# Kernel tuning notes

Measured on AMD Instinct MI355X. Metric: run time of the kernel, lower is better.

Reference implementation:

```python
import jax, jax.numpy as jnp
import numpy as np

N, E = 10000, 160000
DIN, H, DOUT, DE = 128, 256, 256, 32


def _lin(k, din, dout, scale=0.05):
    return jax.random.normal(k, (din, dout), jnp.float32) * scale


def setup_inputs() -> dict:
    key = jax.random.key(0)
    ks = jax.random.split(key, 40)
    inp = {}
    inp["x"] = jax.random.normal(ks[0], (N, DIN), jnp.float32)
    inp["edge_attr"] = jax.random.normal(ks[1], (E, DE), jnp.float32)
    inp["src"] = jax.random.randint(ks[2], (E,), 0, N, jnp.int32)
    inp["dst"] = jax.random.randint(ks[3], (E,), 0, N, jnp.int32)
    # encoders
    inp["W_edge_enc"] = _lin(ks[4], DE, H); inp["b_edge_enc"] = jnp.zeros((H,), jnp.float32)
    inp["W_node_enc"] = _lin(ks[5], DIN, H); inp["b_node_enc"] = jnp.zeros((H,), jnp.float32)
    # 3 TransformerConv layers (heads=1): q,k,v (with bias), edge (no bias), skip (with bias)
    outs = [H, H, DOUT]
    i = 6
    for l, C in enumerate(outs, start=1):
        inp[f"Wq{l}"] = _lin(ks[i], H, C); i += 1
        inp[f"bq{l}"] = jnp.zeros((C,), jnp.float32)
        inp[f"Wk{l}"] = _lin(ks[i], H, C); i += 1
        inp[f"bk{l}"] = jnp.zeros((C,), jnp.float32)
        inp[f"Wv{l}"] = _lin(ks[i], H, C); i += 1
        inp[f"bv{l}"] = jnp.zeros((C,), jnp.float32)
        inp[f"We{l}"] = _lin(ks[i], H, C); i += 1
        inp[f"Ws{l}"] = _lin(ks[i], H, C); i += 1
        inp[f"bs{l}"] = jnp.zeros((C,), jnp.float32)
    return inp


def _tconv(x, src, dst, edge_emb, Wq, bq, Wk, bk, Wv, bv, We, Ws, bs):
    # PyG TransformerConv, heads=1, concat=True, root_weight=True
    n = x.shape[0]
    C = Wq.shape[1]
    q = x @ Wq + bq            # [N, C]
    k = x @ Wk + bk            # [N, C]
    v = x @ Wv + bv            # [N, C]
    e = edge_emb @ We          # [E, C] (lin_edge, no bias)
    kj = k[src] + e            # [E, C]
    alpha = jnp.sum(q[dst] * kj, axis=-1) / jnp.sqrt(jnp.float32(C))  # [E]
    # segment softmax over incoming edges per target node
    m = jax.ops.segment_max(alpha, dst, num_segments=n)
    a = jnp.exp(alpha - m[dst])
    denom = jax.ops.segment_sum(a, dst, num_segments=n)
    a = a / jnp.maximum(denom[dst], 1e-16)
    msg = (v[src] + e) * a[:, None]                       # [E, C]
    out = jax.ops.segment_sum(msg, dst, num_segments=n)   # [N, C]
    return out + x @ Ws + bs                               # root skip


def reference(x, edge_attr, src, dst,
              W_edge_enc, b_edge_enc, W_node_enc, b_node_enc,
              Wq1, bq1, Wk1, bk1, Wv1, bv1, We1, Ws1, bs1,
              Wq2, bq2, Wk2, bk2, Wv2, bv2, We2, Ws2, bs2,
              Wq3, bq3, Wk3, bk3, Wv3, bv3, We3, Ws3, bs3):
    relu = jax.nn.relu
    edge_feat = relu(edge_attr @ W_edge_enc + b_edge_enc)  # [E, H]
    h = relu(x @ W_node_enc + b_node_enc)                  # [N, H]
    # dropout(0.3) is identity in eval mode
    h = relu(_tconv(h, src, dst, edge_feat, Wq1, bq1, Wk1, bk1, Wv1, bv1, We1, Ws1, bs1))
    h = relu(_tconv(h, src, dst, edge_feat, Wq2, bq2, Wk2, bk2, Wv2, bv2, We2, Ws2, bs2))
    h = _tconv(h, src, dst, edge_feat, Wq3, bq3, Wk3, bk3, Wv3, bv3, We3, Ws3, bs3)
    return h
```

## Files before the change

kernel.cpp:

```cpp
#include <hip/hip_runtime.h>
#include <cstdint>

typedef unsigned short u16;
typedef __attribute__((ext_vector_type(8))) short short8;
typedef __attribute__((ext_vector_type(8))) __bf16 bf16x8;
typedef __attribute__((ext_vector_type(4))) float f32x4;

#define DEV __device__ __forceinline__

DEV u16 f2bf(float f){
  uint32_t u = __float_as_uint(f);
  u += 0x7fffu + ((u >> 16) & 1u);
  return (u16)(u >> 16);
}
DEV float bf2f(u16 h){ return __uint_as_float(((uint32_t)h) << 16); }

DEV f32x4 mfma16(short8 a, short8 b, f32x4 c){
  return __builtin_amdgcn_mfma_f32_16x16x32_bf16(
      __builtin_bit_cast(bf16x8, a), __builtin_bit_cast(bf16x8, b), c, 0, 0, 0);
}

#define NN 10000
#define EE 160000
#define MPN 10112
#define MPE 160128

__global__ void count_k(const int* __restrict__ dst, int* __restrict__ cnt){
  int i = blockIdx.x * 256 + threadIdx.x;
  if(i < EE) atomicAdd(&cnt[dst[i]], 1);
}

__global__ void scan1_k(const int* __restrict__ cnt, int* __restrict__ offs,
                        int* __restrict__ bsum){
  __shared__ int buf[256];
  int b = blockIdx.x, tid = threadIdx.x, i = b * 256 + tid;
  int v = (i < NN) ? cnt[i] : 0;
  buf[tid] = v; __syncthreads();
  for(int d = 1; d < 256; d <<= 1){
    int t = (tid >= d) ? buf[tid - d] : 0;
    __syncthreads();
    buf[tid] += t;
    __syncthreads();
  }
  if(i < NN) offs[i] = buf[tid] - v;
  if(tid == 255) bsum[b] = buf[255];
}

__global__ void scan23_k(int* __restrict__ offs, const int* __restrict__ bsum,
                         int* __restrict__ cursor){
  __shared__ int bpre_s;
  int b = blockIdx.x, tid = threadIdx.x;
  if(tid == 0){
    int s = 0;
    for(int i = 0; i < b; ++i) s += bsum[i];
    bpre_s = s;
  }
  __syncthreads();
  int i = b * 256 + tid;
  if(i < NN){ int v = offs[i] + bpre_s; offs[i] = v; cursor[i] = v; }
  if(i == 0) offs[NN] = EE;
}

__global__ void scatter_k(const int* __restrict__ dst, int* __restrict__ cursor,
                          int* __restrict__ eids){
  int i = blockIdx.x * 256 + threadIdx.x;
  if(i < EE){ int p = atomicAdd(&cursor[dst[i]], 1); eids[p] = i; }
}

__global__ void rank_k(const int* __restrict__ dst, const int* __restrict__ src,
                       const int* __restrict__ offs, const int* __restrict__ eids,
                       int* __restrict__ eidp, int* __restrict__ srcp){
  int e = blockIdx.x * 256 + threadIdx.x;
  if(e >= MPE) return;
  if(e >= EE){ eidp[e] = e; return; }
  int n = dst[e];
  int p0 = offs[n], p1 = offs[n + 1];
  int rk = 0;
  for(int p = p0; p < p1; ++p) rk += (eids[p] < e) ? 1 : 0;
  int slot = p0 + rk;
  eidp[slot] = e;
  srcp[slot] = src[e];
}

struct WPack {
  const float* Wq[3]; const float* Wk[3]; const float* Wv[3];
  const float* Ws[3]; const float* We[3];
  const float* bq[3]; const float* bk[3]; const float* bv[3]; const float* bs[3];
};

#define PG0 5056
#define PG1 (PG0 + 20016)
#define PG2 (PG1 + 3840)
#define PG3 (PG2 + 1536)
#define PG4 (PG3 + 15)
#define PG5 (PG4 + 256)

__global__ __launch_bounds__(256) void prep_all_k(
    const float* __restrict__ x, const float* __restrict__ eattr, WPack P,
    const float* __restrict__ Wne, const float* __restrict__ Wee,
    u16* __restrict__ xbf, u16* __restrict__ eabf,
    u16* __restrict__ Wcat, u16* __restrict__ Wet,
    u16* __restrict__ WqBF, u16* __restrict__ WeBF,
    float* __restrict__ biasc, u16* __restrict__ Wnet, u16* __restrict__ Weet)
{
  int b = blockIdx.x, tid = threadIdx.x;
  if(b < PG0){
    int i = b * 256 + tid;
    xbf[i] = (i < NN * 128) ? f2bf(x[i]) : (u16)0;
  } else if(b < PG1){
    int i = (b - PG0) * 256 + tid;
    eabf[i] = (i < EE * 32) ? f2bf(eattr[i]) : (u16)0;
  } else if(b < PG2){
    int b2 = b - PG1; int l = b2 / 1280, r = b2 % 1280; int k = tid;
    float v;
    if(r < 256)       v = P.Wq[l][k * 256 + r];
    else if(r < 512)  v = P.Ws[l][k * 256 + (r - 256)];
    else if(r < 768){ Wet[((size_t)l * 256 + (r - 512)) * 256 + k] =
                        f2bf(P.We[l][k * 256 + (r - 512)]); return; }
    else if(r < 1024) v = P.Wk[l][k * 256 + (r - 768)];
    else              v = P.Wv[l][k * 256 + (r - 1024)];
    Wcat[((size_t)l * 1280 + r) * 256 + k] = f2bf(v);
  } else if(b < PG3){
    int b3 = b - PG2; int l = b3 >> 9, rr = b3 & 511; int t = tid;
    if(rr < 256) WqBF[((size_t)l * 256 + rr) * 256 + t] = f2bf(P.Wq[l][rr * 256 + t]);
    else         WeBF[((size_t)l * 256 + (rr - 256)) * 256 + t] = f2bf(P.We[l][(rr - 256) * 256 + t]);
  } else if(b < PG4){
    int b4 = b - PG3; int l = b4 / 5, seg = b4 % 5; int t = tid;
    float v;
    if(seg == 0)      v = P.bq[l][t];
    else if(seg == 1) v = P.bs[l][t];
    else if(seg == 2){
      const float* we = P.We[l] + (size_t)t * 256; const float* bq = P.bq[l];
      float s = 0.f;
      for(int c = 0; c < 256; ++c) s += bq[c] * we[c];
      v = s;
    }
    else if(seg == 3) v = P.bk[l][t];
    else              v = P.bv[l][t];
    biasc[(size_t)l * 1280 + seg * 256 + t] = v;
  } else {
    int n = b - PG4;
    if(tid < 128) Wnet[n * 128 + tid] = f2bf(Wne[(size_t)tid * 256 + n]);
    if(tid < 32)  Weet[n * 32 + tid]  = f2bf(Wee[(size_t)tid * 256 + n]);
  }
}

template<int BK, int EPI, int AG = 0>
__global__ __launch_bounds__(256) void gemm_k(
    const u16* __restrict__ A, const u16* __restrict__ Bt,
    const float* __restrict__ bias, void* __restrict__ Out,
    const float* __restrict__ accv, const float* __restrict__ skipS,
    const int* __restrict__ rowmap, u16* __restrict__ kvout,
    float* __restrict__ skipOut,
    int Mreal, int Nld, int K, size_t sA, size_t sB, size_t sOb)
{
  constexpr int CPR = BK / 8;
  constexpr int SW  = (BK == 64) ? 7 : 3;
  __shared__ short8 smem8[2048];
  u16* Al = (u16*)smem8;
  u16* Bl = Al + 128 * BK;
  A  += (size_t)blockIdx.z * sA;
  Bt += (size_t)blockIdx.z * sB;
  Out = (void*)((char*)Out + (size_t)blockIdx.z * sOb);
  int tid = threadIdx.x, lane = tid & 63;
  int rowBase = blockIdx.x * 128, colBase = blockIdx.y * 128;
  int wave = tid >> 6, wm = wave >> 1, wn = wave & 1;
  int lr = lane & 15, lk = lane >> 4;
  f32x4 acc[4][4] = {};
  int nkt = K / BK;
  for(int kt = 0; kt < nkt; ++kt){
    __syncthreads();
    for(int ci = tid; ci < 128 * CPR; ci += 256){
      int r = ci / CPR, cb = ci % CPR;
      int ar = AG ? rowmap[rowBase + r] : (rowBase + r);
      int d = (r * CPR + (cb ^ (r & SW))) * 8;
      *(short8*)&Al[d] = *(const short8*)&A [(size_t)ar * K + kt * BK + cb * 8];
      *(short8*)&Bl[d] = *(const short8*)&Bt[(size_t)(colBase + r) * K + kt * BK + cb * 8];
    }
    __syncthreads();
    #pragma unroll
    for(int kk = 0; kk < BK / 32; ++kk){
      short8 af[4], bfr[4];
      #pragma unroll
      for(int m = 0; m < 4; ++m){
        int r = wm * 64 + m * 16 + lr;
        int byt = r * (BK * 2) + kk * 64 + lk * 16; byt ^= (r & SW) << 4;
        af[m] = *(const short8*)((const char*)Al + byt);
      }
      #pragma unroll
      for(int n = 0; n < 4; ++n){
        int r = wn * 64 + n * 16 + lr;
        int byt = r * (BK * 2) + kk * 64 + lk * 16; byt ^= (r & SW) << 4;
        bfr[n] = *(const short8*)((const char*)Bl + byt);
      }
      #pragma unroll
      for(int m = 0; m < 4; ++m)
        #pragma unroll
        for(int n = 0; n < 4; ++n)
          acc[m][n] = mfma16(af[m], bfr[n], acc[m][n]);
    }
  }

  __syncthreads();
  if constexpr(EPI == 0){
    int sec = colBase >> 8;
    if(sec == 1){
      float* fs = (float*)smem8;
      #pragma unroll
      for(int h = 0; h < 2; ++h){
        if(wm == h){
          #pragma unroll
          for(int m = 0; m < 4; ++m)
            #pragma unroll
            for(int n = 0; n < 4; ++n){
              int cc = wn * 64 + n * 16 + lr;
              #pragma unroll
              for(int j = 0; j < 4; ++j){
                int r2 = m * 16 + lk * 4 + j;
                fs[r2 * 128 + cc] = acc[m][n][j] + bias[colBase + cc];
              }
            }
        }
        __syncthreads();
        for(int ch = tid; ch < 2048; ch += 256){
          int rr = ch >> 5, cc = (ch & 31) << 2;
          int r = rowBase + h * 64 + rr;
          if(r < Mreal)
            *(float4*)&skipOut[(size_t)r * 256 + (colBase - 256) + cc] = *(float4*)&fs[rr * 128 + cc];
        }
        __syncthreads();
      }
    } else {
      u16* us = (u16*)smem8;
      #pragma unroll
      for(int m = 0; m < 4; ++m)
        #pragma unroll
        for(int n = 0; n < 4; ++n){
          int cc = wn * 64 + n * 16 + lr;
          #pragma unroll
          for(int j = 0; j < 4; ++j){
            int rr = wm * 64 + m * 16 + lk * 4 + j;
            us[rr * 128 + cc] = f2bf(acc[m][n][j] + bias[colBase + cc]);
          }
        }
      __syncthreads();
      u16* dstp; int cofs;
      if(sec == 0){ dstp = (u16*)Out; cofs = colBase; }
      else if(sec == 2){ dstp = (u16*)Out; cofs = colBase - 256; }
      else { dstp = kvout; cofs = colBase - 768; }
      for(int ch = tid; ch < 2048; ch += 256){
        int rr = ch >> 4, cc = (ch & 15) << 3;
        int r = rowBase + rr;
        if(r < Mreal)
          *(short8*)&dstp[(size_t)r * 512 + cofs + cc] = *(short8*)&us[rr * 128 + cc];
      }
    }
  } else if constexpr(EPI == 4){
    float* fs = (float*)smem8;
    #pragma unroll
    for(int h = 0; h < 2; ++h){
      if(wm == h){
        #pragma unroll
        for(int m = 0; m < 4; ++m)
          #pragma unroll
          for(int n = 0; n < 4; ++n){
            int cc = wn * 64 + n * 16 + lr;
            int c = colBase + cc;
            #pragma unroll
            for(int j = 0; j < 4; ++j){
              int r2 = m * 16 + lk * 4 + j;
              int r = rowBase + h * 64 + r2;
              fs[r2 * 128 + cc] = acc[m][n][j]
                + accv[(size_t)r * 256 + c] + skipS[(size_t)r * 256 + c];
            }
          }
      }
      __syncthreads();
      for(int ch = tid; ch < 2048; ch += 256){
        int rr = ch >> 5, cc = (ch & 31) << 2;
        int r = rowBase + h * 64 + rr;
        if(r < Mreal)
          *(float4*)&((float*)Out)[(size_t)r * Nld + colBase + cc] = *(float4*)&fs[rr * 128 + cc];
      }
      __syncthreads();
    }
  } else {
    u16* us = (u16*)smem8;
    #pragma unroll
    for(int m = 0; m < 4; ++m)
      #pragma unroll
      for(int n = 0; n < 4; ++n){
        int cc = wn * 64 + n * 16 + lr;
        int c = colBase + cc;
        #pragma unroll
        for(int j = 0; j < 4; ++j){
          int rr = wm * 64 + m * 16 + lk * 4 + j;
          float v = acc[m][n][j];
          if constexpr(EPI == 1){ v += bias[c]; v = fmaxf(v, 0.f); }
          else if constexpr(EPI == 3){
            int r = rowBase + rr;
            v += accv[(size_t)r * 256 + c] + skipS[(size_t)r * 256 + c];
            v = fmaxf(v, 0.f);
          }
          us[rr * 128 + cc] = f2bf(v);
        }
      }
    __syncthreads();
    for(int ch = tid; ch < 2048; ch += 256){
      int rr = ch >> 4, cc = (ch & 15) << 3;
      int r = rowBase + rr;
      if(r < Mreal)
        *(short8*)&((u16*)Out)[(size_t)r * Nld + colBase + cc] = *(short8*)&us[rr * 128 + cc];
    }
  }
}

__global__ __launch_bounds__(256) void node_pass_k(
    const u16* __restrict__ qq, const u16* __restrict__ efp,
    const u16* __restrict__ kvbf,
    const int* __restrict__ srcp, const int* __restrict__ offs,
    float* __restrict__ accv, u16* __restrict__ aggef)
{
  int tid = threadIdx.x, lane = tid & 63;
  int li = lane & 15, gb = lane & 48;
  int n = blockIdx.x * 16 + (tid >> 4);
  if(n >= NN) return;
  const u16* qrow = qq + (size_t)n * 512 + li * 16;
  short8 qh0 = *(const short8*)(qrow),       qh1 = *(const short8*)(qrow + 8);
  short8 eh0 = *(const short8*)(qrow + 256), eh1 = *(const short8*)(qrow + 264);
  float q[16], e[16];
  #pragma unroll
  for(int d = 0; d < 8; ++d){
    q[d] = bf2f((u16)qh0[d]); q[8 + d] = bf2f((u16)qh1[d]);
    e[d] = bf2f((u16)eh0[d]); e[8 + d] = bf2f((u16)eh1[d]);
  }
  float av[16], ag[16];
  #pragma unroll
  for(int d = 0; d < 16; ++d){ av[d] = 0.f; ag[d] = 0.f; }
  float den = 0.f;
  int p0 = offs[n], deg = offs[n + 1] - p0;
  for(int base = 0; base < deg; base += 16){
    int scnt = deg - base; if(scnt > 16) scnt = 16;
    int ssrc = (li < scnt) ? srcp[p0 + base + li] : 0;
    int jj = 0;
    for(; jj + 1 < scnt; jj += 2){
      int s1 = __shfl(ssrc, gb + jj);
      int s2 = __shfl(ssrc, gb + jj + 1);
      size_t p1 = (size_t)(p0 + base + jj);
      const u16* kv1 = kvbf + ((size_t)s1 << 9) + li * 16;
      const u16* kv2 = kvbf + ((size_t)s2 << 9) + li * 16;
      const u16* e1 = efp + (p1 << 8) + li * 16;
      const u16* e2 = efp + ((p1 + 1) << 8) + li * 16;
      short8 kA1 = *(const short8*)(kv1),       kB1 = *(const short8*)(kv1 + 8);
      short8 vA1 = *(const short8*)(kv1 + 256), vB1 = *(const short8*)(kv1 + 264);
      short8 fA1 = *(const short8*)(e1),        fB1 = *(const short8*)(e1 + 8);
      short8 kA2 = *(const short8*)(kv2),       kB2 = *(const short8*)(kv2 + 8);
      short8 vA2 = *(const short8*)(kv2 + 256), vB2 = *(const short8*)(kv2 + 264);
      short8 fA2 = *(const short8*)(e2),        fB2 = *(const short8*)(e2 + 8);
      float sc1 = 0.f, sc2 = 0.f;
      #pragma unroll
      for(int d = 0; d < 8; ++d){
        sc1 += q[d]   * bf2f((u16)kA1[d]) + e[d]   * bf2f((u16)fA1[d]);
        sc1 += q[8+d] * bf2f((u16)kB1[d]) + e[8+d] * bf2f((u16)fB1[d]);
        sc2 += q[d]   * bf2f((u16)kA2[d]) + e[d]   * bf2f((u16)fA2[d]);
        sc2 += q[8+d] * bf2f((u16)kB2[d]) + e[8+d] * bf2f((u16)fB2[d]);
      }
      sc1 += __shfl_xor(sc1, 1); sc2 += __shfl_xor(sc2, 1);
      sc1 += __shfl_xor(sc1, 2); sc2 += __shfl_xor(sc2, 2);
      sc1 += __shfl_xor(sc1, 4); sc2 += __shfl_xor(sc2, 4);
      sc1 += __shfl_xor(sc1, 8); sc2 += __shfl_xor(sc2, 8);
      float w1 = __expf(sc1 * 0.0625f);
      float w2 = __expf(sc2 * 0.0625f);
      den += w1 + w2;
      #pragma unroll
      for(int d = 0; d < 8; ++d){
        av[d]   += w1 * bf2f((u16)vA1[d]) + w2 * bf2f((u16)vA2[d]);
        av[8+d] += w1 * bf2f((u16)vB1[d]) + w2 * bf2f((u16)vB2[d]);
        ag[d]   += w1 * bf2f((u16)fA1[d]) + w2 * bf2f((u16)fA2[d]);
        ag[8+d] += w1 * bf2f((u16)fB1[d]) + w2 * bf2f((u16)fB2[d]);
      }
    }
    if(jj < scnt){
      int s = __shfl(ssrc, gb + jj);
      size_t p = (size_t)(p0 + base + jj);
      const u16* kvp = kvbf + ((size_t)s << 9) + li * 16;
      const u16* ep = efp + (p << 8) + li * 16;
      short8 kA = *(const short8*)(kvp),       kB = *(const short8*)(kvp + 8);
      short8 vA = *(const short8*)(kvp + 256), vB = *(const short8*)(kvp + 264);
      short8 fA = *(const short8*)(ep),        fB = *(const short8*)(ep + 8);
      float part = 0.f;
      #pragma unroll
      for(int d = 0; d < 8; ++d){
        part += q[d]   * bf2f((u16)kA[d]) + e[d]   * bf2f((u16)fA[d]);
        part += q[8+d] * bf2f((u16)kB[d]) + e[8+d] * bf2f((u16)fB[d]);
      }
      part += __shfl_xor(part, 1);
      part += __shfl_xor(part, 2);
      part += __shfl_xor(part, 4);
      part += __shfl_xor(part, 8);
      float wgt = __expf(part * 0.0625f);
      den += wgt;
      #pragma unroll
      for(int d = 0; d < 8; ++d){
        av[d]   += wgt * bf2f((u16)vA[d]);
        av[8+d] += wgt * bf2f((u16)vB[d]);
        ag[d]   += wgt * bf2f((u16)fA[d]);
        ag[8+d] += wgt * bf2f((u16)fB[d]);
      }
    }
  }
  float rden = 1.f / fmaxf(den, 1e-16f);
  float* ao = accv + (size_t)n * 256 + li * 16;
  #pragma unroll
  for(int t = 0; t < 4; ++t){
    float4 o;
    o.x = av[t*4+0] * rden; o.y = av[t*4+1] * rden;
    o.z = av[t*4+2] * rden; o.w = av[t*4+3] * rden;
    *(float4*)(ao + t * 4) = o;
  }
  u16* go = aggef + (size_t)n * 256 + li * 16;
  #pragma unroll
  for(int t = 0; t < 2; ++t){
    short8 o;
    #pragma unroll
    for(int d = 0; d < 8; ++d) o[d] = (short)f2bf(ag[t*8+d] * rden);
    *(short8*)(go + t * 8) = o;
  }
}

extern "C" void kernel_launch(void* const* d_in, const int* in_sizes, int n_in,
                              void* d_out, int out_size, void* d_ws, size_t ws_size,
                              hipStream_t stream){
  const float* x     = (const float*)d_in[0];
  const float* eattr = (const float*)d_in[1];
  const int*   src   = (const int*)d_in[2];
  const int*   dst   = (const int*)d_in[3];
  const float* Wee   = (const float*)d_in[4];
  const float* bee   = (const float*)d_in[5];
  const float* Wne   = (const float*)d_in[6];
  const float* bne   = (const float*)d_in[7];
  WPack P;
  for(int l = 0; l < 3; ++l){
    const int b = 8 + l * 9;
    P.Wq[l] = (const float*)d_in[b + 0]; P.bq[l] = (const float*)d_in[b + 1];
    P.Wk[l] = (const float*)d_in[b + 2]; P.bk[l] = (const float*)d_in[b + 3];
    P.Wv[l] = (const float*)d_in[b + 4]; P.bv[l] = (const float*)d_in[b + 5];
    P.We[l] = (const float*)d_in[b + 6];
    P.Ws[l] = (const float*)d_in[b + 7]; P.bs[l] = (const float*)d_in[b + 8];
  }

  char* w = (char*)d_ws; size_t off = 0;
  auto alloc = [&](size_t bytes)->char*{
    char* p = w + off; off = (off + bytes + 255) & ~(size_t)255; return p;
  };
  u16*   Wcat  = (u16*)  alloc((size_t)3 * 1280 * 256 * 2);
  u16*   Wet   = (u16*)  alloc((size_t)3 * 256 * 256 * 2);
  u16*   WqBF  = (u16*)  alloc((size_t)3 * 256 * 256 * 2);
  u16*   WeBF  = (u16*)  alloc((size_t)3 * 256 * 256 * 2);
  float* biasc = (float*)alloc((size_t)3 * 1280 * 4);
  u16*   Wnet  = (u16*)  alloc((size_t)256 * 128 * 2);
  u16*   Weet  = (u16*)  alloc((size_t)256 * 32 * 2);
  u16*   xbf   = (u16*)  alloc((size_t)MPN * 128 * 2);
  u16*   eabf  = (u16*)  alloc((size_t)MPE * 32 * 2);
  u16*   hbf   = (u16*)  alloc((size_t)MPN * 256 * 2);
  u16*   qq    = (u16*)  alloc((size_t)MPN * 512 * 2);
  float* skipf = (float*)alloc((size_t)MPN * 256 * 4);
  u16*   kvbf  = (u16*)  alloc((size_t)MPN * 512 * 2);
  u16*   efp   = (u16*)  alloc((size_t)MPE * 256 * 2);
  int*   cnt   = (int*)  alloc((size_t)NN * 4);
  int*   offs  = (int*)  alloc((size_t)(NN + 1) * 4);
  int*   cursor= (int*)  alloc((size_t)NN * 4);
  int*   bsum  = (int*)  alloc((size_t)64 * 4);
  int*   eids  = (int*)  alloc((size_t)EE * 4);
  int*   eidp  = (int*)  alloc((size_t)MPE * 4);
  int*   srcp  = (int*)  alloc((size_t)EE * 4);
  float* accv  = (float*)alloc((size_t)MPN * 256 * 4);
  u16*   aggef = (u16*)  alloc((size_t)MPN * 256 * 2);
  if(off > ws_size) return;

  hipMemsetAsync(cnt, 0, (size_t)NN * 4, stream);
  count_k <<<(EE + 255) / 256, 256, 0, stream>>>(dst, cnt);
  scan1_k <<<40, 256, 0, stream>>>(cnt, offs, bsum);
  scan23_k<<<40, 256, 0, stream>>>(offs, bsum, cursor);
  scatter_k<<<(EE + 255) / 256, 256, 0, stream>>>(dst, cursor, eids);
  rank_k  <<<(MPE + 255) / 256, 256, 0, stream>>>(dst, src, offs, eids, eidp, srcp);

  prep_all_k<<<PG5, 256, 0, stream>>>(x, eattr, P, Wne, Wee,
      xbf, eabf, Wcat, Wet, WqBF, WeBF, biasc, Wnet, Weet);

  gemm_k<64,5><<<dim3(2, 2, 3), 256, 0, stream>>>(
      WeBF, WqBF, nullptr, Wcat + (size_t)512 * 256,
      nullptr, nullptr, nullptr, nullptr, nullptr, 256, 256, 256,
      (size_t)256 * 256, (size_t)256 * 256, (size_t)1280 * 256 * 2);

  gemm_k<64,1><<<dim3(MPN / 128, 2), 256, 0, stream>>>(
      xbf, Wnet, bne, hbf, nullptr, nullptr, nullptr, nullptr, nullptr,
      NN, 256, 128, 0, 0, 0);
  gemm_k<32,1,1><<<dim3(MPE / 128, 2), 256, 0, stream>>>(
      eabf, Weet, bee, efp, nullptr, nullptr, eidp, nullptr, nullptr,
      EE, 256, 32, 0, 0, 0);

  for(int l = 0; l < 3; ++l){
    gemm_k<64,0><<<dim3(MPN / 128, 10), 256, 0, stream>>>(
        hbf, Wcat + (size_t)l * 1280 * 256, biasc + (size_t)l * 1280, qq,
        nullptr, nullptr, nullptr, kvbf, skipf, NN, 512, 256, 0, 0, 0);
    node_pass_k<<<625, 256, 0, stream>>>(qq, efp, kvbf, srcp, offs, accv, aggef);
    if(l < 2)
      gemm_k<64,3><<<dim3(MPN / 128, 2), 256, 0, stream>>>(
          aggef, Wet + (size_t)l * 256 * 256, nullptr, hbf,
          accv, skipf, nullptr, nullptr, nullptr, NN, 256, 256, 0, 0, 0);
    else
      gemm_k<64,4><<<dim3(MPN / 128, 2), 256, 0, stream>>>(
          aggef, Wet + (size_t)l * 256 * 256, nullptr, d_out,
          accv, skipf, nullptr, nullptr, nullptr, NN, 256, 256, 0, 0, 0);
  }
}
```

Baseline: 359.7 us.

## Fuse CSR build and encoder GEMMs, store intermediates in fp16, widen node pass

Four kernels for CSR counting and scanning become one single-block kernel that builds a histogram and prefix sum in shared memory. The three encoder and weight-fold GEMM launches merge into one kernel. The skip and accumulated-value intermediates are stored as fp16 instead of fp32, which halves their memory traffic. The node pass now uses a full wave per node and splits edges across four lane groups, then reduces them with shuffles. The single-block CSR kernel serialises the histogram over all edges, and fp16 storage loses some precision.

New measurement: 414.0 us. 1.15x slower.

```diff
diff --git a/kernel.cpp b/kernel.cpp
--- a/kernel.cpp
+++ b/kernel.cpp
@@ -14,6 +14,8 @@
   return (u16)(u >> 16);
 }
 DEV float bf2f(u16 h){ return __uint_as_float(((uint32_t)h) << 16); }
+DEV u16 f2h(float f){ return __builtin_bit_cast(u16, (_Float16)f); }
+DEV float h2f(u16 h){ return (float)__builtin_bit_cast(_Float16, h); }
 
 DEV f32x4 mfma16(short8 a, short8 b, f32x4 c){
   return __builtin_amdgcn_mfma_f32_16x16x32_bf16(
@@ -25,40 +27,38 @@
 #define MPN 10112
 #define MPE 160128
 
-__global__ void count_k(const int* __restrict__ dst, int* __restrict__ cnt){
-  int i = blockIdx.x * 256 + threadIdx.x;
-  if(i < EE) atomicAdd(&cnt[dst[i]], 1);
-}
-
-__global__ void scan1_k(const int* __restrict__ cnt, int* __restrict__ offs,
-                        int* __restrict__ bsum){
-  __shared__ int buf[256];
-  int b = blockIdx.x, tid = threadIdx.x, i = b * 256 + tid;
-  int v = (i < NN) ? cnt[i] : 0;
-  buf[tid] = v; __syncthreads();
-  for(int d = 1; d < 256; d <<= 1){
-    int t = (tid >= d) ? buf[tid - d] : 0;
+__global__ __launch_bounds__(1024) void csr1_k(const int* __restrict__ dst,
+                                               int* __restrict__ offs,
+                                               int* __restrict__ cursor){
+  __shared__ int hist[NN];
+  __shared__ int psum[1024];
+  int tid = threadIdx.x;
+  for(int i = tid; i < NN; i += 1024) hist[i] = 0;
+  __syncthreads();
+  for(int i = tid; i < EE; i += 1024) atomicAdd(&hist[dst[i]], 1);
+  __syncthreads();
+  int base = tid * 10;
+  int s = 0;
+  #pragma unroll
+  for(int j = 0; j < 10; ++j){
+    int idx = base + j;
+    if(idx < NN){ int t = hist[idx]; hist[idx] = s; s += t; }
+  }
+  psum[tid] = s;
+  __syncthreads();
+  for(int d = 1; d < 1024; d <<= 1){
+    int t = (tid >= d) ? psum[tid - d] : 0;
     __syncthreads();
-    buf[tid] += t;
+    psum[tid] += t;
     __syncthreads();
   }
-  if(i < NN) offs[i] = buf[tid] - v;
-  if(tid == 255) bsum[b] = buf[255];
-}
-
-__global__ void scan23_k(int* __restrict__ offs, const int* __restrict__ bsum,
-                         int* __restrict__ cursor){
-  __shared__ int bpre_s;
-  int b = blockIdx.x, tid = threadIdx.x;
-  if(tid == 0){
-    int s = 0;
-    for(int i = 0; i < b; ++i) s += bsum[i];
-    bpre_s = s;
-  }
-  __syncthreads();
-  int i = b * 256 + tid;
-  if(i < NN){ int v = offs[i] + bpre_s; offs[i] = v; cursor[i] = v; }
-  if(i == 0) offs[NN] = EE;
+  int add = (tid > 0) ? psum[tid - 1] : 0;
+  #pragma unroll
+  for(int j = 0; j < 10; ++j){
+    int idx = base + j;
+    if(idx < NN){ int v = hist[idx] + add; offs[idx] = v; cursor[idx] = v; }
+  }
+  if(tid == 0) offs[NN] = EE;
 }
 
 __global__ void scatter_k(const int* __restrict__ dst, int* __restrict__ cursor,
@@ -145,25 +145,25 @@
   }
 }
 
-template<int BK, int EPI, int AG = 0>
-__global__ __launch_bounds__(256) void gemm_k(
+template<int BK, int EPI, int AG>
+DEV void gemm_body(short8* smem8,
     const u16* __restrict__ A, const u16* __restrict__ Bt,
-    const float* __restrict__ bias, void* __restrict__ Out,
-    const float* __restrict__ accv, const float* __restrict__ skipS,
+    const float* __restrict__ bias, void* Out,
+    const u16* __restrict__ accvH, const u16* __restrict__ skipH,
     const int* __restrict__ rowmap, u16* __restrict__ kvout,
-    float* __restrict__ skipOut,
+    u16* __restrict__ skipOut,
+    int bx, int by, int bz,
     int Mreal, int Nld, int K, size_t sA, size_t sB, size_t sOb)
 {
   constexpr int CPR = BK / 8;
   constexpr int SW  = (BK == 64) ? 7 : 3;
-  __shared__ short8 smem8[2048];
   u16* Al = (u16*)smem8;
   u16* Bl = Al + 128 * BK;
-  A  += (size_t)blockIdx.z * sA;
-  Bt += (size_t)blockIdx.z * sB;
-  Out = (void*)((char*)Out + (size_t)blockIdx.z * sOb);
+  A  += (size_t)bz * sA;
+  Bt += (size_t)bz * sB;
+  Out = (void*)((char*)Out + (size_t)bz * sOb);
   int tid = threadIdx.x, lane = tid & 63;
-  int rowBase = blockIdx.x * 128, colBase = blockIdx.y * 128;
+  int rowBase = bx * 128, colBase = by * 128;
   int wave = tid >> 6, wm = wave >> 1, wn = wave & 1;
   int lr = lane & 15, lk = lane >> 4;
   f32x4 acc[4][4] = {};
@@ -202,60 +202,7 @@
   }
 
   __syncthreads();
-  if constexpr(EPI == 0){
-    int sec = colBase >> 8;
-    if(sec == 1){
-      float* fs = (float*)smem8;
-      #pragma unroll
-      for(int h = 0; h < 2; ++h){
-        if(wm == h){
-          #pragma unroll
-          for(int m = 0; m < 4; ++m)
-            #pragma unroll
-            for(int n = 0; n < 4; ++n){
-              int cc = wn * 64 + n * 16 + lr;
-              #pragma unroll
-              for(int j = 0; j < 4; ++j){
-                int r2 = m * 16 + lk * 4 + j;
-                fs[r2 * 128 + cc] = acc[m][n][j] + bias[colBase + cc];
-              }
-            }
-        }
-        __syncthreads();
-        for(int ch = tid; ch < 2048; ch += 256){
-          int rr = ch >> 5, cc = (ch & 31) << 2;
-          int r = rowBase + h * 64 + rr;
-          if(r < Mreal)
-            *(float4*)&skipOut[(size_t)r * 256 + (colBase - 256) + cc] = *(float4*)&fs[rr * 128 + cc];
-        }
-        __syncthreads();
-      }
-    } else {
-      u16* us = (u16*)smem8;
-      #pragma unroll
-      for(int m = 0; m < 4; ++m)
-        #pragma unroll
-        for(int n = 0; n < 4; ++n){
-          int cc = wn * 64 + n * 16 + lr;
-          #pragma unroll
-          for(int j = 0; j < 4; ++j){
-            int rr = wm * 64 + m * 16 + lk * 4 + j;
-            us[rr * 128 + cc] = f2bf(acc[m][n][j] + bias[colBase + cc]);
-          }
-        }
-      __syncthreads();
-      u16* dstp; int cofs;
-      if(sec == 0){ dstp = (u16*)Out; cofs = colBase; }
-      else if(sec == 2){ dstp = (u16*)Out; cofs = colBase - 256; }
-      else { dstp = kvout; cofs = colBase - 768; }
-      for(int ch = tid; ch < 2048; ch += 256){
-        int rr = ch >> 4, cc = (ch & 15) << 3;
-        int r = rowBase + rr;
-        if(r < Mreal)
-          *(short8*)&dstp[(size_t)r * 512 + cofs + cc] = *(short8*)&us[rr * 128 + cc];
-      }
-    }
-  } else if constexpr(EPI == 4){
+  if constexpr(EPI == 4){
     float* fs = (float*)smem8;
     #pragma unroll
     for(int h = 0; h < 2; ++h){
@@ -271,7 +218,7 @@
               int r2 = m * 16 + lk * 4 + j;
               int r = rowBase + h * 64 + r2;
               fs[r2 * 128 + cc] = acc[m][n][j]
-                + accv[(size_t)r * 256 + c] + skipS[(size_t)r * 256 + c];
+                + h2f(accvH[(size_t)r * 256 + c]) + h2f(skipH[(size_t)r * 256 + c]);
             }
           }
       }
@@ -283,6 +230,33 @@
           *(float4*)&((float*)Out)[(size_t)r * Nld + colBase + cc] = *(float4*)&fs[rr * 128 + cc];
       }
       __syncthreads();
+    }
+  } else if constexpr(EPI == 0){
+    int sec = by >> 1;
+    u16* us = (u16*)smem8;
+    #pragma unroll
+    for(int m = 0; m < 4; ++m)
+      #pragma unroll
+      for(int n = 0; n < 4; ++n){
+        int cc = wn * 64 + n * 16 + lr;
+        #pragma unroll
+        for(int j = 0; j < 4; ++j){
+          int rr = wm * 64 + m * 16 + lk * 4 + j;
+          float v = acc[m][n][j] + bias[colBase + cc];
+          us[rr * 128 + cc] = (sec == 1) ? f2h(v) : f2bf(v);
+        }
+      }
+    __syncthreads();
+    u16* dstp; int cofs, ldd;
+    if(sec == 0){ dstp = (u16*)Out; cofs = colBase; ldd = 512; }
+    else if(sec == 1){ dstp = skipOut; cofs = colBase - 256; ldd = 256; }
+    else if(sec == 2){ dstp = (u16*)Out; cofs = colBase - 256; ldd = 512; }
+    else { dstp = kvout; cofs = colBase - 768; ldd = 512; }
+    for(int ch = tid; ch < 2048; ch += 256){
+      int rr = ch >> 4, cc = (ch & 15) << 3;
+      int r = rowBase + rr;
+      if(r < Mreal)
+        *(short8*)&dstp[(size_t)r * ldd + cofs + cc] = *(short8*)&us[rr * 128 + cc];
     }
   } else {
     u16* us = (u16*)smem8;
@@ -299,7 +273,7 @@
           if constexpr(EPI == 1){ v += bias[c]; v = fmaxf(v, 0.f); }
           else if constexpr(EPI == 3){
             int r = rowBase + rr;
-            v += accv[(size_t)r * 256 + c] + skipS[(size_t)r * 256 + c];
+            v += h2f(accvH[(size_t)r * 256 + c]) + h2f(skipH[(size_t)r * 256 + c]);
             v = fmaxf(v, 0.f);
           }
           us[rr * 128 + cc] = f2bf(v);
@@ -315,16 +289,64 @@
   }
 }
 
+__global__ __launch_bounds__(256) void slab_k(
+    const u16* __restrict__ A, const u16* __restrict__ Bt,
+    const float* __restrict__ bias, u16* __restrict__ qq,
+    u16* __restrict__ kvout, u16* __restrict__ skipOut){
+  __shared__ short8 smem[2048];
+  gemm_body<64,0,0>(smem, A, Bt, bias, qq, nullptr, nullptr, nullptr, kvout, skipOut,
+                    blockIdx.x, blockIdx.y, 0, NN, 512, 256, 0, 0, 0);
+}
+
+__global__ __launch_bounds__(256) void out3_k(
+    const u16* __restrict__ A, const u16* __restrict__ Bt, u16* __restrict__ Out,
+    const u16* __restrict__ accvH, const u16* __restrict__ skipH){
+  __shared__ short8 smem[2048];
+  gemm_body<64,3,0>(smem, A, Bt, nullptr, Out, accvH, skipH, nullptr, nullptr, nullptr,
+                    blockIdx.x, blockIdx.y, 0, NN, 256, 256, 0, 0, 0);
+}
+
+__global__ __launch_bounds__(256) void out4_k(
+    const u16* __restrict__ A, const u16* __restrict__ Bt, float* __restrict__ Out,
+    const u16* __restrict__ accvH, const u16* __restrict__ skipH){
+  __shared__ short8 smem[2048];
+  gemm_body<64,4,0>(smem, A, Bt, nullptr, Out, accvH, skipH, nullptr, nullptr, nullptr,
+                    blockIdx.x, blockIdx.y, 0, NN, 256, 256, 0, 0, 0);
+}
+
+__global__ __launch_bounds__(256) void enc_all_k(
+    const u16* __restrict__ xbf, const u16* __restrict__ Wnet,
+    const float* __restrict__ bne, u16* __restrict__ hbf,
+    const u16* __restrict__ eabf, const u16* __restrict__ Weet,
+    const float* __restrict__ bee, u16* __restrict__ efp, const int* __restrict__ eidp,
+    const u16* __restrict__ WeBF, const u16* __restrict__ WqBF, u16* __restrict__ WcatQ){
+  __shared__ short8 smem[2048];
+  int b = blockIdx.x;
+  if(b < 158){
+    gemm_body<64,1,0>(smem, xbf, Wnet, bne, hbf, nullptr, nullptr, nullptr, nullptr, nullptr,
+                      b >> 1, b & 1, 0, NN, 256, 128, 0, 0, 0);
+  } else if(b < 2660){
+    int bb = b - 158;
+    gemm_body<32,1,1>(smem, eabf, Weet, bee, efp, nullptr, nullptr, eidp, nullptr, nullptr,
+                      bb >> 1, bb & 1, 0, EE, 256, 32, 0, 0, 0);
+  } else {
+    int bb = b - 2660;
+    gemm_body<64,5,0>(smem, WeBF, WqBF, nullptr, WcatQ, nullptr, nullptr, nullptr, nullptr, nullptr,
+                      bb & 1, (bb >> 1) & 1, bb >> 2, 256, 256, 256,
+                      (size_t)256 * 256, (size_t)256 * 256, (size_t)1280 * 256 * 2);
+  }
+}
+
 __global__ __launch_bounds__(256) void node_pass_k(
     const u16* __restrict__ qq, const u16* __restrict__ efp,
     const u16* __restrict__ kvbf,
     const int* __restrict__ srcp, const int* __restrict__ offs,
-    float* __restrict__ accv, u16* __restrict__ aggef)
+    u16* __restrict__ accvH, u16* __restrict__ aggef)
 {
-  int tid = threadIdx.x, lane = tid & 63;
-  int li = lane & 15, gb = lane & 48;
-  int n = blockIdx.x * 16 + (tid >> 4);
+  int wave = threadIdx.x >> 6, lane = threadIdx.x & 63;
+  int n = blockIdx.x * 4 + wave;
   if(n >= NN) return;
+  int li = lane & 15, eg = lane >> 4, gb = lane & 48;
   const u16* qrow = qq + (size_t)n * 512 + li * 16;
   short8 qh0 = *(const short8*)(qrow),       qh1 = *(const short8*)(qrow + 8);
   short8 eh0 = *(const short8*)(qrow + 256), eh1 = *(const short8*)(qrow + 264);
@@ -339,18 +361,21 @@
   for(int d = 0; d < 16; ++d){ av[d] = 0.f; ag[d] = 0.f; }
   float den = 0.f;
   int p0 = offs[n], deg = offs[n + 1] - p0;
-  for(int base = 0; base < deg; base += 16){
-    int scnt = deg - base; if(scnt > 16) scnt = 16;
-    int ssrc = (li < scnt) ? srcp[p0 + base + li] : 0;
+  int nwin = (deg + 63) >> 6;
+  for(int t = 0; t < nwin; ++t){
+    int gstart = t * 64 + eg * 16;
+    int rem = deg - gstart;
+    int scnt = rem < 16 ? (rem < 0 ? 0 : rem) : 16;
+    int ssrc = (li < scnt) ? srcp[p0 + gstart + li] : 0;
     int jj = 0;
     for(; jj + 1 < scnt; jj += 2){
       int s1 = __shfl(ssrc, gb + jj);
       int s2 = __shfl(ssrc, gb + jj + 1);
-      size_t p1 = (size_t)(p0 + base + jj);
+      size_t pp = (size_t)(p0 + gstart + jj);
       const u16* kv1 = kvbf + ((size_t)s1 << 9) + li * 16;
       const u16* kv2 = kvbf + ((size_t)s2 << 9) + li * 16;
-      const u16* e1 = efp + (p1 << 8) + li * 16;
-      const u16* e2 = efp + ((p1 + 1) << 8) + li * 16;
+      const u16* e1 = efp + (pp << 8) + li * 16;
+      const u16* e2 = efp + ((pp + 1) << 8) + li * 16;
       short8 kA1 = *(const short8*)(kv1),       kB1 = *(const short8*)(kv1 + 8);
       short8 vA1 = *(const short8*)(kv1 + 256), vB1 = *(const short8*)(kv1 + 264);
       short8 fA1 = *(const short8*)(e1),        fB1 = *(const short8*)(e1 + 8);
@@ -382,9 +407,9 @@
     }
     if(jj < scnt){
       int s = __shfl(ssrc, gb + jj);
-      size_t p = (size_t)(p0 + base + jj);
+      size_t pp = (size_t)(p0 + gstart + jj);
       const u16* kvp = kvbf + ((size_t)s << 9) + li * 16;
-      const u16* ep = efp + (p << 8) + li * 16;
+      const u16* ep = efp + (pp << 8) + li * 16;
       short8 kA = *(const short8*)(kvp),       kB = *(const short8*)(kvp + 8);
       short8 vA = *(const short8*)(kvp + 256), vB = *(const short8*)(kvp + 264);
       short8 fA = *(const short8*)(ep),        fB = *(const short8*)(ep + 8);
@@ -409,22 +434,31 @@
       }
     }
   }
+  #pragma unroll
+  for(int d = 0; d < 16; ++d){
+    av[d] += __shfl_xor(av[d], 16); av[d] += __shfl_xor(av[d], 32);
+    ag[d] += __shfl_xor(ag[d], 16); ag[d] += __shfl_xor(ag[d], 32);
+  }
+  den += __shfl_xor(den, 16); den += __shfl_xor(den, 32);
   float rden = 1.f / fmaxf(den, 1e-16f);
-  float* ao = accv + (size_t)n * 256 + li * 16;
-  #pragma unroll
-  for(int t = 0; t < 4; ++t){
-    float4 o;
-    o.x = av[t*4+0] * rden; o.y = av[t*4+1] * rden;
-    o.z = av[t*4+2] * rden; o.w = av[t*4+3] * rden;
-    *(float4*)(ao + t * 4) = o;
-  }
-  u16* go = aggef + (size_t)n * 256 + li * 16;
-  #pragma unroll
-  for(int t = 0; t < 2; ++t){
-    short8 o;
+  if(eg == 0){
+    u16* ao = accvH + (size_t)n * 256 + li * 16;
     #pragma unroll
-    for(int d = 0; d < 8; ++d) o[d] = (short)f2bf(ag[t*8+d] * rden);
-    *(short8*)(go + t * 8) = o;
+    for(int t = 0; t < 2; ++t){
+      short8 o;
+      #pragma unroll
+      for(int d = 0; d < 8; ++d) o[d] = (short)f2h(av[t*8+d] * rden);
+      *(short8*)(ao + t * 8) = o;
+    }
+  } else if(eg == 1){
+    u16* go = aggef + (size_t)n * 256 + li * 16;
+    #pragma unroll
+    for(int t = 0; t < 2; ++t){
+      short8 o;
+      #pragma unroll
+      for(int d = 0; d < 8; ++d) o[d] = (short)f2bf(ag[t*8+d] * rden);
+      *(short8*)(go + t * 8) = o;
+    }
   }
 }
 
@@ -464,54 +498,39 @@
   u16*   eabf  = (u16*)  alloc((size_t)MPE * 32 * 2);
   u16*   hbf   = (u16*)  alloc((size_t)MPN * 256 * 2);
   u16*   qq    = (u16*)  alloc((size_t)MPN * 512 * 2);
-  float* skipf = (float*)alloc((size_t)MPN * 256 * 4);
+  u16*   skipf = (u16*)  alloc((size_t)MPN * 256 * 2);
   u16*   kvbf  = (u16*)  alloc((size_t)MPN * 512 * 2);
   u16*   efp   = (u16*)  alloc((size_t)MPE * 256 * 2);
-  int*   cnt   = (int*)  alloc((size_t)NN * 4);
   int*   offs  = (int*)  alloc((size_t)(NN + 1) * 4);
   int*   cursor= (int*)  alloc((size_t)NN * 4);
-  int*   bsum  = (int*)  alloc((size_t)64 * 4);
   int*   eids  = (int*)  alloc((size_t)EE * 4);
   int*   eidp  = (int*)  alloc((size_t)MPE * 4);
   int*   srcp  = (int*)  alloc((size_t)EE * 4);
-  float* accv  = (float*)alloc((size_t)MPN * 256 * 4);
+  u16*   accv  = (u16*)  alloc((size_t)MPN * 256 * 2);
   u16*   aggef = (u16*)  alloc((size_t)MPN * 256 * 2);
   if(off > ws_size) return;
 
-  hipMemsetAsync(cnt, 0, (size_t)NN * 4, stream);
-  count_k <<<(EE + 255) / 256, 256, 0, stream>>>(dst, cnt);
-  scan1_k <<<40, 256, 0, stream>>>(cnt, offs, bsum);
-  scan23_k<<<40, 256, 0, stream>>>(offs, bsum, cursor);
+  csr1_k  <<<1, 1024, 0, stream>>>(dst, offs, cursor);
   scatter_k<<<(EE + 255) / 256, 256, 0, stream>>>(dst, cursor, eids);
   rank_k  <<<(MPE + 255) / 256, 256, 0, stream>>>(dst, src, offs, eids, eidp, srcp);
 
   prep_all_k<<<PG5, 256, 0, stream>>>(x, eattr, P, Wne, Wee,
       xbf, eabf, Wcat, Wet, WqBF, WeBF, biasc, Wnet, Weet);
 
-  gemm_k<64,5><<<dim3(2, 2, 3), 256, 0, stream>>>(
-      WeBF, WqBF, nullptr, Wcat + (size_t)512 * 256,
-      nullptr, nullptr, nullptr, nullptr, nullptr, 256, 256, 256,
-      (size_t)256 * 256, (size_t)256 * 256, (size_t)1280 * 256 * 2);
-
-  gemm_k<64,1><<<dim3(MPN / 128, 2), 256, 0, stream>>>(
-      xbf, Wnet, bne, hbf, nullptr, nullptr, nullptr, nullptr, nullptr,
-      NN, 256, 128, 0, 0, 0);
-  gemm_k<32,1,1><<<dim3(MPE / 128, 2), 256, 0, stream>>>(
-      eabf, Weet, bee, efp, nullptr, nullptr, eidp, nullptr, nullptr,
-      EE, 256, 32, 0, 0, 0);
+  enc_all_k<<<2672, 256, 0, stream>>>(
+      xbf, Wnet, bne, hbf,
+      eabf, Weet, bee, efp, eidp,
+      WeBF, WqBF, Wcat + (size_t)512 * 256);
 
   for(int l = 0; l < 3; ++l){
-    gemm_k<64,0><<<dim3(MPN / 128, 10), 256, 0, stream>>>(
-        hbf, Wcat + (size_t)l * 1280 * 256, biasc + (size_t)l * 1280, qq,
-        nullptr, nullptr, nullptr, kvbf, skipf, NN, 512, 256, 0, 0, 0);
-    node_pass_k<<<625, 256, 0, stream>>>(qq, efp, kvbf, srcp, offs, accv, aggef);
+    slab_k<<<dim3(MPN / 128, 10), 256, 0, stream>>>(
+        hbf, Wcat + (size_t)l * 1280 * 256, biasc + (size_t)l * 1280, qq, kvbf, skipf);
+    node_pass_k<<<NN / 4, 256, 0, stream>>>(qq, efp, kvbf, srcp, offs, accv, aggef);
     if(l < 2)
-      gemm_k<64,3><<<dim3(MPN / 128, 2), 256, 0, stream>>>(
-          aggef, Wet + (size_t)l * 256 * 256, nullptr, hbf,
-          accv, skipf, nullptr, nullptr, nullptr, NN, 256, 256, 0, 0, 0);
+      out3_k<<<dim3(MPN / 128, 2), 256, 0, stream>>>(
+          aggef, Wet + (size_t)l * 256 * 256, hbf, accv, skipf);
     else
-      gemm_k<64,4><<<dim3(MPN / 128, 2), 256, 0, stream>>>(
-          aggef, Wet + (size_t)l * 256 * 256, nullptr, d_out,
-          accv, skipf, nullptr, nullptr, nullptr, NN, 256, 256, 0, 0, 0);
-  }
-}
+      out4_k<<<dim3(MPN / 128, 2), 256, 0, stream>>>(
+          aggef, Wet + (size_t)l * 256 * 256, (float*)d_out, accv, skipf);
+  }
+}
```
